# Optimization experiments

Measured on AMD Instinct MI355X. Metric: run time of the kernel, lower is better.

## Reference

```python
import jax, jax.numpy as jnp
import numpy as np

GAMMA = 1.0
ALPHA = 0.5
EPS = 1e-8


def setup_inputs() -> dict:
    key = jax.random.key(0)
    k1, k2 = jax.random.split(key)
    x = jax.random.normal(k1, (2048, 32), dtype=jnp.float32)
    y = jax.random.normal(k2, (2048, 32), dtype=jnp.float32)
    return {"x": x, "y": y}


def _normalize(a):
    # torch: mean/std over batch dim, std is unbiased (ddof=1)
    mu = jnp.mean(a, axis=0, keepdims=True)
    sd = jnp.std(a, axis=0, ddof=1, keepdims=True)
    return (a - mu) / (sd + EPS)


def reference(x, y):
    # Classical RBF kernel on normalized inputs
    xn = _normalize(x)
    yn = _normalize(y)
    d = xn[:, None, :] - yn[None, :, :]            # [N, M, D]
    classical = jnp.exp(-GAMMA * jnp.sum(d * d, axis=-1))  # [N, M]

    # Quantum kernel, analytic closed form:
    # RY(t)|0> = [cos(t/2), sin(t/2)]; product state overlap ->
    # |<psi_x|psi_y>|^2 = prod_i cos^2((x_i - y_i)/2)
    qd = (x[:, None, :] - y[None, :, :]) * 0.5     # [N, M, D]
    quantum = jnp.prod(jnp.square(jnp.cos(qd)), axis=-1)    # [N, M]

    return (1.0 - ALPHA) * classical + ALPHA * quantum
```

## Files before the change

### kernel.cpp

```cpp
#include <hip/hip_runtime.h>
#include <math.h>

#define NROWS 2048
#define DDIM 32

typedef __attribute__((ext_vector_type(8))) short short8;
typedef __attribute__((ext_vector_type(4))) float f32x4;

__device__ __forceinline__ unsigned packbf(float a, float b) {
  return (__float_as_uint(a) >> 16) | (__float_as_uint(b) & 0xffff0000u);
}

__global__ __launch_bounds__(512, 2) void HybridKernel_fused(
    const float* __restrict__ x, const float* __restrict__ y,
    float* __restrict__ out) {
  __shared__ float4 sCS[2][16 * 128];
  __shared__ uint4 sXB[2][2][128 * 5];
  __shared__ float4 sRed[2][64][8];
  __shared__ float4 sRedQ[2][64][8];
  __shared__ float sNrm[2][128];
  __shared__ float sMu[2][32];
  __shared__ float sInv[2][32];

  const int t = threadIdx.x;
  const int i0 = blockIdx.y * 128;
  const int j0 = blockIdx.x * 128;

  float4 gx[2], gy[2];
#pragma unroll
  for (int rep = 0; rep < 2; ++rep) {
    const int u = t + 512 * rep;
    const int row = u >> 3;
    const int q = u & 7;
    gx[rep] = *reinterpret_cast<const float4*>(&x[(i0 + row) * DDIM + q * 4]);
    gy[rep] = *reinterpret_cast<const float4*>(&y[(j0 + row) * DDIM + q * 4]);
  }

#pragma unroll
  for (int rep = 0; rep < 2; ++rep) {
    const int u = t + 512 * rep;
    const int row = u >> 3;
    const int q = u & 7;
#pragma unroll
    for (int side = 0; side < 2; ++side) {
      const float4 g = side ? gy[rep] : gx[rep];
      const float sc = side ? 1.0f : 0.5f;
      const float gv[4] = {g.x, g.y, g.z, g.w};
      float hc[4], hs[4];
#pragma unroll
      for (int k = 0; k < 4; ++k) {
        float sn, cs;
        __sincosf(gv[k], &sn, &cs);
        hc[k] = sc * cs;
        hs[k] = sc * sn;
      }
      const int dp0 = 2 * q, dp1 = 2 * q + 1;
      sCS[side][dp0 * 128 + (row ^ (dp0 & 7))] =
          make_float4(hc[0], hs[0], hc[1], hs[1]);
      sCS[side][dp1 * 128 + (row ^ (dp1 & 7))] =
          make_float4(hc[2], hs[2], hc[3], hs[3]);
    }
  }

  {
    const int cq = t & 7;
    const int rg = t >> 3;
    const float4* px = reinterpret_cast<const float4*>(x) + rg * 8 + cq;
    const float4* py = reinterpret_cast<const float4*>(y) + rg * 8 + cq;
    float4 sx = {0.f, 0.f, 0.f, 0.f}, qx = {0.f, 0.f, 0.f, 0.f};
    float4 sy = {0.f, 0.f, 0.f, 0.f}, qy = {0.f, 0.f, 0.f, 0.f};
#pragma unroll 4
    for (int i = 0; i < NROWS / 64; ++i) {
      const float4 vx = px[(size_t)i * 64 * 8];
      const float4 vy = py[(size_t)i * 64 * 8];
      sx.x += vx.x; qx.x = fmaf(vx.x, vx.x, qx.x);
      sx.y += vx.y; qx.y = fmaf(vx.y, vx.y, qx.y);
      sx.z += vx.z; qx.z = fmaf(vx.z, vx.z, qx.z);
      sx.w += vx.w; qx.w = fmaf(vx.w, vx.w, qx.w);
      sy.x += vy.x; qy.x = fmaf(vy.x, vy.x, qy.x);
      sy.y += vy.y; qy.y = fmaf(vy.y, vy.y, qy.y);
      sy.z += vy.z; qy.z = fmaf(vy.z, vy.z, qy.z);
      sy.w += vy.w; qy.w = fmaf(vy.w, vy.w, qy.w);
    }
    sRed[0][rg][cq] = sx;
    sRedQ[0][rg][cq] = qx;
    sRed[1][rg][cq] = sy;
    sRedQ[1][rg][cq] = qy;
  }
  __syncthreads();
  if (t < 128) {
    const int a = t >> 6;
    const int g8 = (t >> 3) & 7;
    const int cq = t & 7;
    float4 S = {0.f, 0.f, 0.f, 0.f}, Q = {0.f, 0.f, 0.f, 0.f};
#pragma unroll
    for (int k = 0; k < 8; ++k) {
      const float4 a1 = sRed[a][g8 * 8 + k][cq];
      const float4 b1 = sRedQ[a][g8 * 8 + k][cq];
      S.x += a1.x; S.y += a1.y; S.z += a1.z; S.w += a1.w;
      Q.x += b1.x; Q.y += b1.y; Q.z += b1.z; Q.w += b1.w;
    }
    sRed[a][g8][cq] = S;
    sRedQ[a][g8][cq] = Q;
  }
  __syncthreads();
  if (t < 16) {
    const int a = t >> 3;
    const int cq = t & 7;
    float4 S = {0.f, 0.f, 0.f, 0.f}, Q = {0.f, 0.f, 0.f, 0.f};
#pragma unroll
    for (int k = 0; k < 8; ++k) {
      const float4 a1 = sRed[a][k][cq];
      const float4 b1 = sRedQ[a][k][cq];
      S.x += a1.x; S.y += a1.y; S.z += a1.z; S.w += a1.w;
      Q.x += b1.x; Q.y += b1.y; Q.z += b1.z; Q.w += b1.w;
    }
    const float Sa[4] = {S.x, S.y, S.z, S.w};
    const float Qa[4] = {Q.x, Q.y, Q.z, Q.w};
    const float n = (float)NROWS;
#pragma unroll
    for (int k = 0; k < 4; ++k) {
      const float mean = Sa[k] / n;
      const float var = fmaxf((Qa[k] - Sa[k] * mean) / (n - 1.f), 0.f);
      sMu[a][cq * 4 + k] = mean;
      sInv[a][cq * 4 + k] = 1.f / (sqrtf(var) + 1e-8f);
    }
  }
  __syncthreads();

#pragma unroll
  for (int rep = 0; rep < 2; ++rep) {
    const int u = t + 512 * rep;
    const int row = u >> 3;
    const int q = u & 7;
#pragma unroll
    for (int side = 0; side < 2; ++side) {
      const float4 g = side ? gy[rep] : gx[rep];
      const float gv[4] = {g.x, g.y, g.z, g.w};
      float xn[4];
      float nrm = 0.f;
#pragma unroll
      for (int k = 0; k < 4; ++k) {
        const int d = q * 4 + k;
        xn[k] = (gv[k] - sMu[side][d]) * sInv[side][d];
        nrm = fmaf(xn[k], xn[k], nrm);
      }
      float hif[4], lof[4];
#pragma unroll
      for (int k = 0; k < 4; ++k) {
        hif[k] = __uint_as_float(__float_as_uint(xn[k]) & 0xffff0000u);
        lof[k] = xn[k] - hif[k];
      }
      char* bh = (char*)&sXB[side][0][0] + row * 80 + q * 8;
      char* bl = (char*)&sXB[side][1][0] + row * 80 + q * 8;
      *reinterpret_cast<uint2*>(bh) =
          make_uint2(packbf(hif[0], hif[1]), packbf(hif[2], hif[3]));
      *reinterpret_cast<uint2*>(bl) =
          make_uint2(packbf(lof[0], lof[1]), packbf(lof[2], lof[3]));
      nrm += __shfl_xor(nrm, 1);
      nrm += __shfl_xor(nrm, 2);
      nrm += __shfl_xor(nrm, 4);
      if ((t & 7) == 0) sNrm[side][row] = nrm;
    }
  }
  __syncthreads();

  const int w = t >> 6;
  const int l = t & 63;
  const int l4 = l >> 4;
  const int ln = l & 15;
  const int R0 = (w >> 1) * 32;
  const int C0 = (w & 1) * 64;

  short8 Ah[2], Al[2], Bh[4], Bl[4];
  {
    const char* bxh = (const char*)&sXB[0][0][0];
    const char* bxl = (const char*)&sXB[0][1][0];
    const char* byh = (const char*)&sXB[1][0][0];
    const char* byl = (const char*)&sXB[1][1][0];
#pragma unroll
    for (int tr = 0; tr < 2; ++tr) {
      const int off = (R0 + 16 * tr + ln) * 80 + l4 * 16;
      Ah[tr] = *reinterpret_cast<const short8*>(bxh + off);
      Al[tr] = *reinterpret_cast<const short8*>(bxl + off);
    }
#pragma unroll
    for (int tc = 0; tc < 4; ++tc) {
      const int off = (C0 + 16 * tc + ln) * 80 + l4 * 16;
      Bh[tc] = *reinterpret_cast<const short8*>(byh + off);
      Bl[tc] = *reinterpret_cast<const short8*>(byl + off);
    }
  }
  f32x4 dotacc[2][4];
#pragma unroll
  for (int tr = 0; tr < 2; ++tr)
#pragma unroll
    for (int tc = 0; tc < 4; ++tc) {
      f32x4 a = {0.f, 0.f, 0.f, 0.f};
      a = __builtin_amdgcn_mfma_f32_16x16x32_bf16(Ah[tr], Bl[tc], a, 0, 0, 0);
      a = __builtin_amdgcn_mfma_f32_16x16x32_bf16(Al[tr], Bh[tc], a, 0, 0, 0);
      a = __builtin_amdgcn_mfma_f32_16x16x32_bf16(Ah[tr], Bh[tc], a, 0, 0, 0);
      dotacc[tr][tc] = a;
    }

  int r_idx[8], c_idx[4];
#pragma unroll
  for (int ri = 0; ri < 8; ++ri)
    r_idx[ri] = R0 + 16 * (ri >> 2) + 4 * l4 + (ri & 3);
#pragma unroll
  for (int tc = 0; tc < 4; ++tc) c_idx[tc] = C0 + 16 * tc + ln;

  float cl[8][4];
#pragma unroll
  for (int tr = 0; tr < 2; ++tr) {
#pragma unroll
    for (int mm = 0; mm < 4; ++mm) {
      const float nx = sNrm[0][r_idx[tr * 4 + mm]];
#pragma unroll
      for (int tc = 0; tc < 4; ++tc) {
        const float ny = sNrm[1][c_idx[tc]];
        cl[tr * 4 + mm][tc] = __expf(2.f * dotacc[tr][tc][mm] - nx - ny);
      }
    }
  }

  const float4* sCS0 = &sCS[0][0];
  const float4* sCS1 = &sCS[1][0];
  float qp[8][4];
#pragma unroll
  for (int ri = 0; ri < 8; ++ri)
#pragma unroll
    for (int tc = 0; tc < 4; ++tc) qp[ri][tc] = 1.f;

#pragma unroll
  for (int dp = 0; dp < 16; ++dp) {
    const int sw = dp & 7;
    float4 FX[8], FY[4];
#pragma unroll
    for (int ri = 0; ri < 8; ++ri) FX[ri] = sCS0[dp * 128 + (r_idx[ri] ^ sw)];
#pragma unroll
    for (int tc = 0; tc < 4; ++tc) FY[tc] = sCS1[dp * 128 + (c_idx[tc] ^ sw)];
#pragma unroll
    for (int ri = 0; ri < 8; ++ri)
#pragma unroll
      for (int tc = 0; tc < 4; ++tc) {
        const float t0 =
            fmaf(FX[ri].x, FY[tc].x, fmaf(FX[ri].y, FY[tc].y, 0.5f));
        const float t1 =
            fmaf(FX[ri].z, FY[tc].z, fmaf(FX[ri].w, FY[tc].w, 0.5f));
        qp[ri][tc] *= t0 * t1;
      }
  }

#pragma unroll
  for (int ri = 0; ri < 8; ++ri) {
    float* o = out + (size_t)(i0 + r_idx[ri]) * NROWS + j0;
#pragma unroll
    for (int tc = 0; tc < 4; ++tc) {
      o[c_idx[tc]] = 0.5f * (cl[ri][tc] + qp[ri][tc]);
    }
  }
}

extern "C" void kernel_launch(void* const* d_in, const int* in_sizes, int n_in,
                              void* d_out, int out_size, void* d_ws,
                              size_t ws_size, hipStream_t stream) {
  const float* x = (const float*)d_in[0];
  const float* y = (const float*)d_in[1];
  float* out = (float*)d_out;

  dim3 grid(NROWS / 128, NROWS / 128);
  HybridKernel_fused<<<grid, 512, 0, stream>>>(x, y, out);
}
```

Baseline: 24.26 us.

## Overlap column-statistics global loads with quantum product loop

Moves the quantum cos-product computation ahead of the normalization statistics and interleaves the full-column sum and sum-of-squares loads into that loop. Each dp iteration issues the global loads for two row groups, so their latency can hide behind the LDS-heavy product arithmetic. The classical exp is then computed and stored directly in the epilogue without a separate cl array. The trade-offs are an extra barrier before the loop, a non-unrolled loop with global loads inside, and register pressure from keeping the accumulators live alongside qp.

```diff
diff --git a/kernel.cpp b/kernel.cpp
--- a/kernel.cpp
+++ b/kernel.cpp
@@ -61,57 +61,111 @@
           make_float4(hc[2], hs[2], hc[3], hs[3]);
     }
   }
-
-  {
-    const int cq = t & 7;
-    const int rg = t >> 3;
-    const float4* px = reinterpret_cast<const float4*>(x) + rg * 8 + cq;
-    const float4* py = reinterpret_cast<const float4*>(y) + rg * 8 + cq;
-    float4 sx = {0.f, 0.f, 0.f, 0.f}, qx = {0.f, 0.f, 0.f, 0.f};
-    float4 sy = {0.f, 0.f, 0.f, 0.f}, qy = {0.f, 0.f, 0.f, 0.f};
-#pragma unroll 4
-    for (int i = 0; i < NROWS / 64; ++i) {
-      const float4 vx = px[(size_t)i * 64 * 8];
-      const float4 vy = py[(size_t)i * 64 * 8];
-      sx.x += vx.x; qx.x = fmaf(vx.x, vx.x, qx.x);
-      sx.y += vx.y; qx.y = fmaf(vx.y, vx.y, qx.y);
-      sx.z += vx.z; qx.z = fmaf(vx.z, vx.z, qx.z);
-      sx.w += vx.w; qx.w = fmaf(vx.w, vx.w, qx.w);
-      sy.x += vy.x; qy.x = fmaf(vy.x, vy.x, qy.x);
-      sy.y += vy.y; qy.y = fmaf(vy.y, vy.y, qy.y);
-      sy.z += vy.z; qy.z = fmaf(vy.z, vy.z, qy.z);
-      sy.w += vy.w; qy.w = fmaf(vy.w, vy.w, qy.w);
-    }
-    sRed[0][rg][cq] = sx;
-    sRedQ[0][rg][cq] = qx;
-    sRed[1][rg][cq] = sy;
-    sRedQ[1][rg][cq] = qy;
-  }
+  __syncthreads();
+
+  const int w = t >> 6;
+  const int l = t & 63;
+  const int l4 = l >> 4;
+  const int ln = l & 15;
+  const int R0 = (w >> 1) * 32;
+  const int C0 = (w & 1) * 64;
+
+  int r_idx[8], c_idx[4];
+#pragma unroll
+  for (int ri = 0; ri < 8; ++ri)
+    r_idx[ri] = R0 + 16 * (ri >> 2) + 4 * l4 + (ri & 3);
+#pragma unroll
+  for (int tc = 0; tc < 4; ++tc) c_idx[tc] = C0 + 16 * tc + ln;
+
+  const int cq = t & 7;
+  const int rg = t >> 3;
+  const float4* pxp = reinterpret_cast<const float4*>(x) + rg * 8 + cq;
+  const float4* pyp = reinterpret_cast<const float4*>(y) + rg * 8 + cq;
+  float4 sxA = {0.f, 0.f, 0.f, 0.f}, qxA = {0.f, 0.f, 0.f, 0.f};
+  float4 syA = {0.f, 0.f, 0.f, 0.f}, qyA = {0.f, 0.f, 0.f, 0.f};
+
+  const float4* sCS0 = &sCS[0][0];
+  const float4* sCS1 = &sCS[1][0];
+  float qp[8][4];
+#pragma unroll
+  for (int ri = 0; ri < 8; ++ri)
+#pragma unroll
+    for (int tc = 0; tc < 4; ++tc) qp[ri][tc] = 1.f;
+
+#pragma unroll 1
+  for (int dp = 0; dp < 16; ++dp) {
+    const float4 vx0 = pxp[0];
+    const float4 vx1 = pxp[512];
+    const float4 vy0 = pyp[0];
+    const float4 vy1 = pyp[512];
+    pxp += 1024;
+    pyp += 1024;
+
+    const int sw = dp & 7;
+    const int base = dp * 128;
+    float4 FX[8], FY[4];
+#pragma unroll
+    for (int ri = 0; ri < 8; ++ri) FX[ri] = sCS0[base + (r_idx[ri] ^ sw)];
+#pragma unroll
+    for (int tc = 0; tc < 4; ++tc) FY[tc] = sCS1[base + (c_idx[tc] ^ sw)];
+#pragma unroll
+    for (int ri = 0; ri < 8; ++ri)
+#pragma unroll
+      for (int tc = 0; tc < 4; ++tc) {
+        const float t0 =
+            fmaf(FX[ri].x, FY[tc].x, fmaf(FX[ri].y, FY[tc].y, 0.5f));
+        const float t1 =
+            fmaf(FX[ri].z, FY[tc].z, fmaf(FX[ri].w, FY[tc].w, 0.5f));
+        qp[ri][tc] *= t0 * t1;
+      }
+
+    sxA.x += vx0.x; qxA.x = fmaf(vx0.x, vx0.x, qxA.x);
+    sxA.y += vx0.y; qxA.y = fmaf(vx0.y, vx0.y, qxA.y);
+    sxA.z += vx0.z; qxA.z = fmaf(vx0.z, vx0.z, qxA.z);
+    sxA.w += vx0.w; qxA.w = fmaf(vx0.w, vx0.w, qxA.w);
+    sxA.x += vx1.x; qxA.x = fmaf(vx1.x, vx1.x, qxA.x);
+    sxA.y += vx1.y; qxA.y = fmaf(vx1.y, vx1.y, qxA.y);
+    sxA.z += vx1.z; qxA.z = fmaf(vx1.z, vx1.z, qxA.z);
+    sxA.w += vx1.w; qxA.w = fmaf(vx1.w, vx1.w, qxA.w);
+    syA.x += vy0.x; qyA.x = fmaf(vy0.x, vy0.x, qyA.x);
+    syA.y += vy0.y; qyA.y = fmaf(vy0.y, vy0.y, qyA.y);
+    syA.z += vy0.z; qyA.z = fmaf(vy0.z, vy0.z, qyA.z);
+    syA.w += vy0.w; qyA.w = fmaf(vy0.w, vy0.w, qyA.w);
+    syA.x += vy1.x; qyA.x = fmaf(vy1.x, vy1.x, qyA.x);
+    syA.y += vy1.y; qyA.y = fmaf(vy1.y, vy1.y, qyA.y);
+    syA.z += vy1.z; qyA.z = fmaf(vy1.z, vy1.z, qyA.z);
+    syA.w += vy1.w; qyA.w = fmaf(vy1.w, vy1.w, qyA.w);
+  }
+
+  sRed[0][rg][cq] = sxA;
+  sRedQ[0][rg][cq] = qxA;
+  sRed[1][rg][cq] = syA;
+  sRedQ[1][rg][cq] = qyA;
   __syncthreads();
   if (t < 128) {
     const int a = t >> 6;
     const int g8 = (t >> 3) & 7;
-    const int cq = t & 7;
+    const int cq2 = t & 7;
     float4 S = {0.f, 0.f, 0.f, 0.f}, Q = {0.f, 0.f, 0.f, 0.f};
 #pragma unroll
     for (int k = 0; k < 8; ++k) {
-      const float4 a1 = sRed[a][g8 * 8 + k][cq];
-      const float4 b1 = sRedQ[a][g8 * 8 + k][cq];
+      const float4 a1 = sRed[a][g8 * 8 + k][cq2];
+      const float4 b1 = sRedQ[a][g8 * 8 + k][cq2];
       S.x += a1.x; S.y += a1.y; S.z += a1.z; S.w += a1.w;
       Q.x += b1.x; Q.y += b1.y; Q.z += b1.z; Q.w += b1.w;
     }
-    sRed[a][g8][cq] = S;
-    sRedQ[a][g8][cq] = Q;
+    sRed[a][g8][cq2] = S;
+    sRedQ[a][g8][cq2] = Q;
   }
   __syncthreads();
   if (t < 16) {
     const int a = t >> 3;
-    const int cq = t & 7;
+    const int cq2 = t & 7;
     float4 S = {0.f, 0.f, 0.f, 0.f}, Q = {0.f, 0.f, 0.f, 0.f};
 #pragma unroll
     for (int k = 0; k < 8; ++k) {
-      const float4 a1 = sRed[a][k][cq];
-      const float4 b1 = sRedQ[a][k][cq];
+      const float4 a1 = sRed[a][k][cq2];
+      const float4 b1 = sRedQ[a][k][cq2];
       S.x += a1.x; S.y += a1.y; S.z += a1.z; S.w += a1.w;
       Q.x += b1.x; Q.y += b1.y; Q.z += b1.z; Q.w += b1.w;
     }
@@ -122,8 +176,8 @@
     for (int k = 0; k < 4; ++k) {
       const float mean = Sa[k] / n;
       const float var = fmaxf((Qa[k] - Sa[k] * mean) / (n - 1.f), 0.f);
-      sMu[a][cq * 4 + k] = mean;
-      sInv[a][cq * 4 + k] = 1.f / (sqrtf(var) + 1e-8f);
+      sMu[a][cq2 * 4 + k] = mean;
+      sInv[a][cq2 * 4 + k] = 1.f / (sqrtf(var) + 1e-8f);
     }
   }
   __syncthreads();
@@ -165,13 +219,6 @@
   }
   __syncthreads();
 
-  const int w = t >> 6;
-  const int l = t & 63;
-  const int l4 = l >> 4;
-  const int ln = l & 15;
-  const int R0 = (w >> 1) * 32;
-  const int C0 = (w & 1) * 64;
-
   short8 Ah[2], Al[2], Bh[4], Bl[4];
   {
     const char* bxh = (const char*)&sXB[0][0][0];
@@ -203,61 +250,19 @@
       dotacc[tr][tc] = a;
     }
 
-  int r_idx[8], c_idx[4];
-#pragma unroll
-  for (int ri = 0; ri < 8; ++ri)
-    r_idx[ri] = R0 + 16 * (ri >> 2) + 4 * l4 + (ri & 3);
-#pragma unroll
-  for (int tc = 0; tc < 4; ++tc) c_idx[tc] = C0 + 16 * tc + ln;
-
-  float cl[8][4];
 #pragma unroll
   for (int tr = 0; tr < 2; ++tr) {
 #pragma unroll
     for (int mm = 0; mm < 4; ++mm) {
-      const float nx = sNrm[0][r_idx[tr * 4 + mm]];
+      const int ri = tr * 4 + mm;
+      const float nx = sNrm[0][r_idx[ri]];
+      float* o = out + (size_t)(i0 + r_idx[ri]) * NROWS + j0;
 #pragma unroll
       for (int tc = 0; tc < 4; ++tc) {
         const float ny = sNrm[1][c_idx[tc]];
-        cl[tr * 4 + mm][tc] = __expf(2.f * dotacc[tr][tc][mm] - nx - ny);
-      }
-    }
-  }
-
-  const float4* sCS0 = &sCS[0][0];
-  const float4* sCS1 = &sCS[1][0];
-  float qp[8][4];
-#pragma unroll
-  for (int ri = 0; ri < 8; ++ri)
-#pragma unroll
-    for (int tc = 0; tc < 4; ++tc) qp[ri][tc] = 1.f;
-
-#pragma unroll
-  for (int dp = 0; dp < 16; ++dp) {
-    const int sw = dp & 7;
-    float4 FX[8], FY[4];
-#pragma unroll
-    for (int ri = 0; ri < 8; ++ri) FX[ri] = sCS0[dp * 128 + (r_idx[ri] ^ sw)];
-#pragma unroll
-    for (int tc = 0; tc < 4; ++tc) FY[tc] = sCS1[dp * 128 + (c_idx[tc] ^ sw)];
-#pragma unroll
-    for (int ri = 0; ri < 8; ++ri)
-#pragma unroll
-      for (int tc = 0; tc < 4; ++tc) {
-        const float t0 =
-            fmaf(FX[ri].x, FY[tc].x, fmaf(FX[ri].y, FY[tc].y, 0.5f));
-        const float t1 =
-            fmaf(FX[ri].z, FY[tc].z, fmaf(FX[ri].w, FY[tc].w, 0.5f));
-        qp[ri][tc] *= t0 * t1;
-      }
-  }
-
-#pragma unroll
-  for (int ri = 0; ri < 8; ++ri) {
-    float* o = out + (size_t)(i0 + r_idx[ri]) * NROWS + j0;
-#pragma unroll
-    for (int tc = 0; tc < 4; ++tc) {
-      o[c_idx[tc]] = 0.5f * (cl[ri][tc] + qp[ri][tc]);
+        const float cl = __expf(2.f * dotacc[tr][tc][mm] - nx - ny);
+        o[c_idx[tc]] = 0.5f * (cl + qp[ri][tc]);
+      }
     }
   }
 }
```

Result: no change. 24.61 us (+1.4%).

## Repack y sin/cos table for packed-FP32 math in quantum product loop

Applied to the files above, without the earlier changes.

Stores the y-side cos/sin values in a new shared-memory layout where pairs of columns sit next to each other. The quantum product loop can then use two-wide vector FMAs, which can map to packed FP32 instructions on CDNA3/4. The exp and classical terms are moved into the final store loop, and the statistics reduction is rewritten with vector types. This aims to halve the VALU instruction count of the dominant product loop. In exchange it uses more scattered scalar LDS writes during setup and a more complex indexing scheme.

```diff
diff --git a/kernel.cpp b/kernel.cpp
--- a/kernel.cpp
+++ b/kernel.cpp
@@ -6,6 +6,7 @@
 
 typedef __attribute__((ext_vector_type(8))) short short8;
 typedef __attribute__((ext_vector_type(4))) float f32x4;
+typedef __attribute__((ext_vector_type(2))) float f32x2;
 
 __device__ __forceinline__ unsigned packbf(float a, float b) {
   return (__float_as_uint(a) >> 16) | (__float_as_uint(b) & 0xffff0000u);
@@ -14,10 +15,11 @@
 __global__ __launch_bounds__(512, 2) void HybridKernel_fused(
     const float* __restrict__ x, const float* __restrict__ y,
     float* __restrict__ out) {
-  __shared__ float4 sCS[2][16 * 128];
+  __shared__ f32x4 sCSx[16 * 128];
+  __shared__ f32x4 sYP[2048];
   __shared__ uint4 sXB[2][2][128 * 5];
-  __shared__ float4 sRed[2][64][8];
-  __shared__ float4 sRedQ[2][64][8];
+  __shared__ f32x4 sRed[2][64][8];
+  __shared__ f32x4 sRedQ[2][64][8];
   __shared__ float sNrm[2][128];
   __shared__ float sMu[2][32];
   __shared__ float sInv[2][32];
@@ -41,46 +43,64 @@
     const int u = t + 512 * rep;
     const int row = u >> 3;
     const int q = u & 7;
-#pragma unroll
-    for (int side = 0; side < 2; ++side) {
-      const float4 g = side ? gy[rep] : gx[rep];
-      const float sc = side ? 1.0f : 0.5f;
+    {
+      const float4 g = gx[rep];
       const float gv[4] = {g.x, g.y, g.z, g.w};
       float hc[4], hs[4];
 #pragma unroll
       for (int k = 0; k < 4; ++k) {
         float sn, cs;
         __sincosf(gv[k], &sn, &cs);
-        hc[k] = sc * cs;
-        hs[k] = sc * sn;
+        hc[k] = 0.5f * cs;
+        hs[k] = 0.5f * sn;
       }
       const int dp0 = 2 * q, dp1 = 2 * q + 1;
-      sCS[side][dp0 * 128 + (row ^ (dp0 & 7))] =
-          make_float4(hc[0], hs[0], hc[1], hs[1]);
-      sCS[side][dp1 * 128 + (row ^ (dp1 & 7))] =
-          make_float4(hc[2], hs[2], hc[3], hs[3]);
+      sCSx[dp0 * 128 + (row ^ (dp0 & 7))] = f32x4{hc[0], hs[0], hc[1], hs[1]};
+      sCSx[dp1 * 128 + (row ^ (dp1 & 7))] = f32x4{hc[2], hs[2], hc[3], hs[3]};
+    }
+    {
+      const float4 g = gy[rep];
+      const float gv[4] = {g.x, g.y, g.z, g.w};
+      float hc[4], hs[4];
+#pragma unroll
+      for (int k = 0; k < 4; ++k) {
+        float sn, cs;
+        __sincosf(gv[k], &sn, &cs);
+        hc[k] = cs;
+        hs[k] = sn;
+      }
+      const int gblk = row >> 5;
+      const int h = (row >> 4) & 1;
+      const int p = row & 15;
+#pragma unroll
+      for (int e = 0; e < 2; ++e) {
+        const int dp = 2 * q + e;
+        const int pp = p ^ dp;
+        float* bA = (float*)&sYP[(dp * 8 + 2 * gblk + 0) * 16 + pp];
+        float* bB = (float*)&sYP[(dp * 8 + 2 * gblk + 1) * 16 + pp];
+        bA[h] = hc[2 * e];
+        bA[2 + h] = hs[2 * e];
+        bB[h] = hc[2 * e + 1];
+        bB[2 + h] = hs[2 * e + 1];
+      }
     }
   }
 
   {
     const int cq = t & 7;
     const int rg = t >> 3;
-    const float4* px = reinterpret_cast<const float4*>(x) + rg * 8 + cq;
-    const float4* py = reinterpret_cast<const float4*>(y) + rg * 8 + cq;
-    float4 sx = {0.f, 0.f, 0.f, 0.f}, qx = {0.f, 0.f, 0.f, 0.f};
-    float4 sy = {0.f, 0.f, 0.f, 0.f}, qy = {0.f, 0.f, 0.f, 0.f};
+    const f32x4* px = reinterpret_cast<const f32x4*>(x) + rg * 8 + cq;
+    const f32x4* py = reinterpret_cast<const f32x4*>(y) + rg * 8 + cq;
+    f32x4 sx = {0.f, 0.f, 0.f, 0.f}, qx = {0.f, 0.f, 0.f, 0.f};
+    f32x4 sy = {0.f, 0.f, 0.f, 0.f}, qy = {0.f, 0.f, 0.f, 0.f};
 #pragma unroll 4
     for (int i = 0; i < NROWS / 64; ++i) {
-      const float4 vx = px[(size_t)i * 64 * 8];
-      const float4 vy = py[(size_t)i * 64 * 8];
-      sx.x += vx.x; qx.x = fmaf(vx.x, vx.x, qx.x);
-      sx.y += vx.y; qx.y = fmaf(vx.y, vx.y, qx.y);
-      sx.z += vx.z; qx.z = fmaf(vx.z, vx.z, qx.z);
-      sx.w += vx.w; qx.w = fmaf(vx.w, vx.w, qx.w);
-      sy.x += vy.x; qy.x = fmaf(vy.x, vy.x, qy.x);
-      sy.y += vy.y; qy.y = fmaf(vy.y, vy.y, qy.y);
-      sy.z += vy.z; qy.z = fmaf(vy.z, vy.z, qy.z);
-      sy.w += vy.w; qy.w = fmaf(vy.w, vy.w, qy.w);
+      const f32x4 vx = px[(size_t)i * 64 * 8];
+      const f32x4 vy = py[(size_t)i * 64 * 8];
+      sx += vx;
+      qx = __builtin_elementwise_fma(vx, vx, qx);
+      sy += vy;
+      qy = __builtin_elementwise_fma(vy, vy, qy);
     }
     sRed[0][rg][cq] = sx;
     sRedQ[0][rg][cq] = qx;
@@ -91,39 +111,33 @@
   if (t < 128) {
     const int a = t >> 6;
     const int g8 = (t >> 3) & 7;
-    const int cq = t & 7;
-    float4 S = {0.f, 0.f, 0.f, 0.f}, Q = {0.f, 0.f, 0.f, 0.f};
+    const int cq2 = t & 7;
+    f32x4 S = {0.f, 0.f, 0.f, 0.f}, Q = {0.f, 0.f, 0.f, 0.f};
 #pragma unroll
     for (int k = 0; k < 8; ++k) {
-      const float4 a1 = sRed[a][g8 * 8 + k][cq];
-      const float4 b1 = sRedQ[a][g8 * 8 + k][cq];
-      S.x += a1.x; S.y += a1.y; S.z += a1.z; S.w += a1.w;
-      Q.x += b1.x; Q.y += b1.y; Q.z += b1.z; Q.w += b1.w;
-    }
-    sRed[a][g8][cq] = S;
-    sRedQ[a][g8][cq] = Q;
+      S += sRed[a][g8 * 8 + k][cq2];
+      Q += sRedQ[a][g8 * 8 + k][cq2];
+    }
+    sRed[a][g8][cq2] = S;
+    sRedQ[a][g8][cq2] = Q;
   }
   __syncthreads();
   if (t < 16) {
     const int a = t >> 3;
-    const int cq = t & 7;
-    float4 S = {0.f, 0.f, 0.f, 0.f}, Q = {0.f, 0.f, 0.f, 0.f};
+    const int cq2 = t & 7;
+    f32x4 S = {0.f, 0.f, 0.f, 0.f}, Q = {0.f, 0.f, 0.f, 0.f};
 #pragma unroll
     for (int k = 0; k < 8; ++k) {
-      const float4 a1 = sRed[a][k][cq];
-      const float4 b1 = sRedQ[a][k][cq];
-      S.x += a1.x; S.y += a1.y; S.z += a1.z; S.w += a1.w;
-      Q.x += b1.x; Q.y += b1.y; Q.z += b1.z; Q.w += b1.w;
-    }
-    const float Sa[4] = {S.x, S.y, S.z, S.w};
-    const float Qa[4] = {Q.x, Q.y, Q.z, Q.w};
+      S += sRed[a][k][cq2];
+      Q += sRedQ[a][k][cq2];
+    }
     const float n = (float)NROWS;
 #pragma unroll
     for (int k = 0; k < 4; ++k) {
-      const float mean = Sa[k] / n;
-      const float var = fmaxf((Qa[k] - Sa[k] * mean) / (n - 1.f), 0.f);
-      sMu[a][cq * 4 + k] = mean;
-      sInv[a][cq * 4 + k] = 1.f / (sqrtf(var) + 1e-8f);
+      const float mean = S[k] / n;
+      const float var = fmaxf((Q[k] - S[k] * mean) / (n - 1.f), 0.f);
+      sMu[a][cq2 * 4 + k] = mean;
+      sInv[a][cq2 * 4 + k] = 1.f / (sqrtf(var) + 1e-8f);
     }
   }
   __syncthreads();
@@ -172,6 +186,13 @@
   const int R0 = (w >> 1) * 32;
   const int C0 = (w & 1) * 64;
 
+  int r_idx[8], c_idx[4];
+#pragma unroll
+  for (int ri = 0; ri < 8; ++ri)
+    r_idx[ri] = R0 + 16 * (ri >> 2) + 4 * l4 + (ri & 3);
+#pragma unroll
+  for (int tc = 0; tc < 4; ++tc) c_idx[tc] = C0 + 16 * tc + ln;
+
   short8 Ah[2], Al[2], Bh[4], Bl[4];
   {
     const char* bxh = (const char*)&sXB[0][0][0];
@@ -203,61 +224,53 @@
       dotacc[tr][tc] = a;
     }
 
-  int r_idx[8], c_idx[4];
-#pragma unroll
-  for (int ri = 0; ri < 8; ++ri)
-    r_idx[ri] = R0 + 16 * (ri >> 2) + 4 * l4 + (ri & 3);
-#pragma unroll
-  for (int tc = 0; tc < 4; ++tc) c_idx[tc] = C0 + 16 * tc + ln;
-
-  float cl[8][4];
+  const int gBase = C0 >> 5;
+  f32x2 qp01[8], qp23[8];
+#pragma unroll
+  for (int ri = 0; ri < 8; ++ri) {
+    qp01[ri] = f32x2{1.f, 1.f};
+    qp23[ri] = f32x2{1.f, 1.f};
+  }
+
+#pragma unroll
+  for (int dp = 0; dp < 16; ++dp) {
+    const int swx = dp & 7;
+    const int pp = ln ^ dp;
+    const f32x4 A0 = sYP[(dp * 8 + 2 * gBase + 0) * 16 + pp];
+    const f32x4 B0 = sYP[(dp * 8 + 2 * gBase + 1) * 16 + pp];
+    const f32x4 A1 = sYP[(dp * 8 + 2 * (gBase + 1) + 0) * 16 + pp];
+    const f32x4 B1 = sYP[(dp * 8 + 2 * (gBase + 1) + 1) * 16 + pp];
+    const f32x2 h2 = {0.5f, 0.5f};
+#pragma unroll
+    for (int ri = 0; ri < 8; ++ri) {
+      const f32x4 fx = sCSx[dp * 128 + (r_idx[ri] ^ swx)];
+      f32x2 i0 = __builtin_elementwise_fma(fx.yy, A0.zw, h2);
+      f32x2 t0 = __builtin_elementwise_fma(fx.xx, A0.xy, i0);
+      f32x2 i1 = __builtin_elementwise_fma(fx.ww, B0.zw, h2);
+      f32x2 t1 = __builtin_elementwise_fma(fx.zz, B0.xy, i1);
+      qp01[ri] *= t0 * t1;
+      f32x2 i2 = __builtin_elementwise_fma(fx.yy, A1.zw, h2);
+      f32x2 t2 = __builtin_elementwise_fma(fx.xx, A1.xy, i2);
+      f32x2 i3 = __builtin_elementwise_fma(fx.ww, B1.zw, h2);
+      f32x2 t3 = __builtin_elementwise_fma(fx.zz, B1.xy, i3);
+      qp23[ri] *= t2 * t3;
+    }
+  }
+
 #pragma unroll
   for (int tr = 0; tr < 2; ++tr) {
 #pragma unroll
     for (int mm = 0; mm < 4; ++mm) {
-      const float nx = sNrm[0][r_idx[tr * 4 + mm]];
+      const int ri = tr * 4 + mm;
+      const float nx = sNrm[0][r_idx[ri]];
+      float* o = out + (size_t)(i0 + r_idx[ri]) * NROWS + j0;
 #pragma unroll
       for (int tc = 0; tc < 4; ++tc) {
         const float ny = sNrm[1][c_idx[tc]];
-        cl[tr * 4 + mm][tc] = __expf(2.f * dotacc[tr][tc][mm] - nx - ny);
-      }
-    }
-  }
-
-  const float4* sCS0 = &sCS[0][0];
-  const float4* sCS1 = &sCS[1][0];
-  float qp[8][4];
-#pragma unroll
-  for (int ri = 0; ri < 8; ++ri)
-#pragma unroll
-    for (int tc = 0; tc < 4; ++tc) qp[ri][tc] = 1.f;
-
-#pragma unroll
-  for (int dp = 0; dp < 16; ++dp) {
-    const int sw = dp & 7;
-    float4 FX[8], FY[4];
-#pragma unroll
-    for (int ri = 0; ri < 8; ++ri) FX[ri] = sCS0[dp * 128 + (r_idx[ri] ^ sw)];
-#pragma unroll
-    for (int tc = 0; tc < 4; ++tc) FY[tc] = sCS1[dp * 128 + (c_idx[tc] ^ sw)];
-#pragma unroll
-    for (int ri = 0; ri < 8; ++ri)
-#pragma unroll
-      for (int tc = 0; tc < 4; ++tc) {
-        const float t0 =
-            fmaf(FX[ri].x, FY[tc].x, fmaf(FX[ri].y, FY[tc].y, 0.5f));
-        const float t1 =
-            fmaf(FX[ri].z, FY[tc].z, fmaf(FX[ri].w, FY[tc].w, 0.5f));
-        qp[ri][tc] *= t0 * t1;
-      }
-  }
-
-#pragma unroll
-  for (int ri = 0; ri < 8; ++ri) {
-    float* o = out + (size_t)(i0 + r_idx[ri]) * NROWS + j0;
-#pragma unroll
-    for (int tc = 0; tc < 4; ++tc) {
-      o[c_idx[tc]] = 0.5f * (cl[ri][tc] + qp[ri][tc]);
+        const float cl = __expf(2.f * dotacc[tr][tc][mm] - nx - ny);
+        const float qv = (tc < 2) ? qp01[ri][tc] : qp23[ri][tc - 2];
+        o[c_idx[tc]] = 0.5f * (cl + qv);
+      }
     }
   }
 }
```

New measurement: 24.78 us. 2.1% more time.
